# Optimization experiments

Measured on AMD Instinct MI355X. Metric: run time of the kernel, lower is better.

## Reference

```python
import jax, jax.numpy as jnp
import numpy as np

VOCAB, P, K, B, L, R = 50257, 512, 64, 32, 2048, 5


def setup_inputs() -> dict:
    key = jax.random.key(0)
    k1, k2, k3, k4, k5, k6, k7 = jax.random.split(key, 7)
    return {
        "x": jax.random.randint(k1, (B, L), 0, VOCAB, dtype=jnp.int32),
        "V": jax.random.normal(k2, (VOCAB, P), dtype=jnp.float32),
        "C": jax.random.normal(k3, (K, P), dtype=jnp.float32),
        "f1_w": jax.random.normal(k4, (2 * R + 1,), dtype=jnp.float32),
        "f1_b": jax.random.normal(k5, (K,), dtype=jnp.float32),
        "f2_w": jax.random.normal(k6, (K, P), dtype=jnp.float32),
        "f2_b": jax.random.normal(k7, (K,), dtype=jnp.float32),
    }


def reference(x, V, C, f1_w, f1_b, f2_w, f2_b):
    b, l = x.shape
    k, p = C.shape
    w = f1_w.shape[0]
    r = (w - 1) // 2
    emb = V[x]                                              # [B,L,P] embedding lookup
    x_hat = emb / jnp.linalg.norm(emb, axis=2, keepdims=True)
    l_hat = C / jnp.linalg.norm(C, axis=1, keepdims=True)
    G = jnp.einsum('kp,blp->bkl', l_hat, x_hat)             # cosine sim [B,K,L]
    # sliding-window dot product == depthwise 1D cross-correlation, 'same' padding
    u = jax.lax.conv_general_dilated(
        G.reshape(b * k, 1, l), f1_w.reshape(1, 1, w),
        window_strides=(1,), padding=[(r, r)],
        dimension_numbers=('NCH', 'OIH', 'NCH'),
    ).reshape(b, k, l)
    m = jax.nn.relu(u + f1_b[None, :, None])                # [B,K,L]
    beta = jax.nn.softmax(m.max(axis=1), axis=1)            # max over labels, softmax over seq -> [B,L]
    pooled = jnp.mean(beta[:, :, None] * emb, axis=1)       # [B,P]
    return pooled @ f2_w.T + f2_b                           # [B,K]
```

## Files before the change

kernel.cpp:

```cpp
#include <hip/hip_runtime.h>
#include <hip/hip_bf16.h>

#define PP     512
#define KK     64
#define BB     32
#define LLEN   2048
#define NPOS   (BB * LLEN)

typedef __attribute__((ext_vector_type(8)))  short short8;
typedef __attribute__((ext_vector_type(16))) float float16;

__device__ inline unsigned int pack_bf2(float lo, float hi) {
    __hip_bfloat162 h = __float22bfloat162_rn(make_float2(lo, hi));
    unsigned int u;
    __builtin_memcpy(&u, &h, 4);
    return u;
}
__device__ inline float bf_lo(unsigned int v) { return __uint_as_float(v << 16); }
__device__ inline float bf_hi(unsigned int v) { return __uint_as_float(v & 0xffff0000u); }

__global__ void k1_prep(const float* __restrict__ C, const float* __restrict__ f2w,
                        ushort* __restrict__ Bu) {
    const int n = blockIdx.x;
    const float* src = (n < 64) ? (C + n * PP) : (f2w + (n - 64) * PP);
    const int t = threadIdx.x;
    float v0 = src[t];
    float v1 = src[t + 256];
    __shared__ float red[256];
    red[t] = v0 * v0 + v1 * v1;
    __syncthreads();
    for (int s = 128; s > 0; s >>= 1) {
        if (t < s) red[t] += red[t + s];
        __syncthreads();
    }
    const float inv = (n < 64) ? rsqrtf(red[0]) : 1.f;
    Bu[(((t >> 3)      * 128 + n) << 3) + (t & 7)] = (ushort)(pack_bf2(v0 * inv, 0.f) & 0xffffu);
    Bu[((((t + 256) >> 3)) * 128 + n) * 8 + (t & 7)] = (ushort)(pack_bf2(v1 * inv, 0.f) & 0xffffu);
}

__launch_bounds__(256, 3)
__global__ void k2_gemm(const int* __restrict__ x, const float* __restrict__ V,
                        const uint4* __restrict__ Bu4,
                        unsigned int* __restrict__ Gt2, unsigned int* __restrict__ E2p) {
    __shared__ uint4 sA[64 * 16];
    __shared__ uint4 sB[16 * 128];
    __shared__ int   stok[64];
    __shared__ float rnorm[64];

    const int tid  = threadIdx.x;
    const int lane = tid & 63;
    const int wv   = tid >> 6;

    if (tid < 64) stok[tid] = x[blockIdx.x * 64 + tid];

    float16 acc0, acc1;
#pragma unroll
    for (int i = 0; i < 16; ++i) { acc0[i] = 0.f; acc1[i] = 0.f; }
    float nacc[4];
#pragma unroll
    for (int i = 0; i < 4; ++i) nacc[i] = 0.f;

    const int mt = (wv & 1) * 32;
    const int nh = (wv >> 1) * 64;

    for (int kc = 0; kc < 4; ++kc) {
        __syncthreads();
#pragma unroll
        for (int i = 0; i < 4; ++i) {
            const int m = (tid >> 4) + i * 16;
            const int f = tid & 15;
            const float* src = V + (size_t)stok[m] * PP + kc * 128 + f * 8;
            const float4 a = ((const float4*)src)[0];
            const float4 b = ((const float4*)src)[1];
            uint4 wq;
            wq.x = pack_bf2(a.x, a.y); wq.y = pack_bf2(a.z, a.w);
            wq.z = pack_bf2(b.x, b.y); wq.w = pack_bf2(b.z, b.w);
            sA[m * 16 + (f ^ (m & 7))] = wq;
            float s2 = 0.f;
            s2 = fmaf(a.x, a.x, s2); s2 = fmaf(a.y, a.y, s2);
            s2 = fmaf(a.z, a.z, s2); s2 = fmaf(a.w, a.w, s2);
            s2 = fmaf(b.x, b.x, s2); s2 = fmaf(b.y, b.y, s2);
            s2 = fmaf(b.z, b.z, s2); s2 = fmaf(b.w, b.w, s2);
            nacc[i] += s2;
        }
#pragma unroll
        for (int i = 0; i < 8; ++i)
            sB[i * 256 + tid] = Bu4[kc * 2048 + i * 256 + tid];

        if (kc == 3) {
#pragma unroll
            for (int i = 0; i < 4; ++i) {
                float r = nacc[i];
                r += __shfl_down(r, 8, 16);
                r += __shfl_down(r, 4, 16);
                r += __shfl_down(r, 2, 16);
                r += __shfl_down(r, 1, 16);
                if ((tid & 15) == 0) rnorm[(tid >> 4) + i * 16] = rsqrtf(r);
            }
        }
        __syncthreads();

#pragma unroll
        for (int kb = 0; kb < 8; ++kb) {
            const int f  = kb * 2 + (lane >> 5);
            const int mq = mt + (lane & 31);
            const uint4 av = sA[mq * 16 + (f ^ (mq & 7))];
            const uint4 b0 = sB[f * 128 + nh + (lane & 31)];
            const uint4 b1 = sB[f * 128 + nh + 32 + (lane & 31)];
            short8 a8, t0, t1;
            __builtin_memcpy(&a8, &av, 16);
            __builtin_memcpy(&t0, &b0, 16);
            __builtin_memcpy(&t1, &b1, 16);
            acc0 = __builtin_amdgcn_mfma_f32_32x32x16_bf16(a8, t0, acc0, 0, 0, 0);
            acc1 = __builtin_amdgcn_mfma_f32_32x32x16_bf16(a8, t1, acc1, 0, 0, 0);
        }
    }

    const size_t posBase = (size_t)blockIdx.x * 64;
#pragma unroll
    for (int reg = 0; reg < 16; ++reg) {
        const int r  = (reg & 3) + 8 * (reg >> 2) + 4 * (lane >> 5);
        const int mq = mt + r;
        const size_t p = posBase + mq;
        if (wv < 2) {
            const float rn = rnorm[mq];
            Gt2[p * 32 + (lane & 31)] = pack_bf2(acc0[reg] * rn, acc1[reg] * rn);
        } else {
            E2p[p * 32 + (lane & 31)] = pack_bf2(acc0[reg], acc1[reg]);
        }
    }
}

__global__ void k3_convmax(const unsigned int* __restrict__ Gt2, const float* __restrict__ f1w,
                           const float* __restrict__ f1b, float* __restrict__ mm) {
    __shared__ unsigned int sT[138 * 33];
    const int b  = blockIdx.x >> 4;
    const int l0 = (blockIdx.x & 15) * 128;
    const int t  = threadIdx.x;
    for (int idx = t; idx < 138 * 32; idx += 256) {
        const int row = idx >> 5, col = idx & 31;
        const int gl = l0 - 5 + row;
        sT[row * 33 + col] = (gl >= 0 && gl < LLEN)
            ? Gt2[((size_t)b * LLEN + gl) * 32 + col] : 0u;
    }
    __syncthreads();
    float w[11];
#pragma unroll
    for (int j = 0; j < 11; ++j) w[j] = f1w[j];
    const int j = t & 31;
    const int h = t >> 5;
    const float bias0 = f1b[j], bias1 = f1b[j + 32];
#pragma unroll 2
    for (int i = 0; i < 16; ++i) {
        const int lr = i * 8 + h;
        float u0 = 0.f, u1 = 0.f;
#pragma unroll
        for (int tap = 0; tap < 11; ++tap) {
            const unsigned int v = sT[(lr + tap) * 33 + j];
            u0 = fmaf(bf_lo(v), w[tap], u0);
            u1 = fmaf(bf_hi(v), w[tap], u1);
        }
        float m = fmaxf(fmaxf(u0 + bias0, 0.f), fmaxf(u1 + bias1, 0.f));
#pragma unroll
        for (int off = 16; off > 0; off >>= 1)
            m = fmaxf(m, __shfl_xor(m, off, 64));
        if (j == 0) mm[b * LLEN + l0 + lr] = m;
    }
}

__global__ void k7_softpool(const float* __restrict__ mm, const unsigned int* __restrict__ E2p,
                            const float* __restrict__ f2b, float* __restrict__ out) {
    const int b = blockIdx.x;
    const int t = threadIdx.x;
    __shared__ float red[256];
    __shared__ float sbeta[LLEN];
    __shared__ float sred[8][64];

    float v[8];
    float mx = -1e30f;
#pragma unroll
    for (int i = 0; i < 8; ++i) {
        v[i] = mm[b * LLEN + t + i * 256];
        mx = fmaxf(mx, v[i]);
    }
    red[t] = mx;
    __syncthreads();
    for (int s = 128; s > 0; s >>= 1) {
        if (t < s) red[t] = fmaxf(red[t], red[t + s]);
        __syncthreads();
    }
    mx = red[0];
    __syncthreads();
    float sm = 0.f;
#pragma unroll
    for (int i = 0; i < 8; ++i) {
        v[i] = __expf(v[i] - mx);
        sm += v[i];
    }
    red[t] = sm;
    __syncthreads();
    for (int s = 128; s > 0; s >>= 1) {
        if (t < s) red[t] += red[t + s];
        __syncthreads();
    }
    const float inv = 1.f / red[0];
#pragma unroll
    for (int i = 0; i < 8; ++i) sbeta[t + i * 256] = v[i] * inv;
    __syncthreads();

    const int j = t & 31, h = t >> 5;
    float a0 = 0.f, a1 = 0.f;
#pragma unroll 8
    for (int i = 0; i < 256; ++i) {
        const int l = i * 8 + h;
        const float wgt = sbeta[l];
        const unsigned int e = E2p[((size_t)b * LLEN + l) * 32 + j];
        a0 = fmaf(wgt, bf_lo(e), a0);
        a1 = fmaf(wgt, bf_hi(e), a1);
    }
    sred[h][j]      = a0;
    sred[h][j + 32] = a1;
    __syncthreads();
    if (t < 64) {
        float r = 0.f;
#pragma unroll
        for (int hh = 0; hh < 8; ++hh) r += sred[hh][t];
        out[b * KK + t] = r * (1.f / 2048.f) + f2b[t];
    }
}

extern "C" void kernel_launch(void* const* d_in, const int* in_sizes, int n_in,
                              void* d_out, int out_size, void* d_ws, size_t ws_size,
                              hipStream_t stream) {
    const int*   x   = (const int*)d_in[0];
    const float* V   = (const float*)d_in[1];
    const float* C   = (const float*)d_in[2];
    const float* f1w = (const float*)d_in[3];
    const float* f1b = (const float*)d_in[4];
    const float* f2w = (const float*)d_in[5];
    const float* f2b = (const float*)d_in[6];
    float* out = (float*)d_out;

    float* ws = (float*)d_ws;
    ushort* Bu = (ushort*)ws;
    unsigned int* Gt2 = (unsigned int*)(ws + 32768);
    unsigned int* E2p = Gt2 + (size_t)NPOS * 32;
    float* mm = (float*)(E2p + (size_t)NPOS * 32);

    k1_prep    <<<128, 256, 0, stream>>>(C, f2w, Bu);
    k2_gemm    <<<NPOS / 64, 256, 0, stream>>>(x, V, (const uint4*)Bu, Gt2, E2p);
    k3_convmax <<<BB * (LLEN / 128), 256, 0, stream>>>(Gt2, f1w, f1b, mm);
    k7_softpool<<<BB, 256, 0, stream>>>(mm, E2p, f2b, out);
}
```

Before: 200.6 us.

## Fuse softmax-pooling into conv kernel with split softmax and prefetch gather rows

The per-batch softmax and weighted pooling move into the conv/max kernel. Each 128-position chunk computes a local max, a local exp-sum and a partial pooled vector, and a small final kernel merges the chunks with rescaled online-softmax. This replaces the 32-block pooling kernel that streamed all of E2p serially with work spread over 512 blocks. The GEMM kernel also register-prefetches the next K-chunk of the gathered V rows before the MFMA loop, which overlaps the global gather with compute at the cost of extra registers.

```diff
diff --git a/kernel.cpp b/kernel.cpp
--- a/kernel.cpp
+++ b/kernel.cpp
@@ -34,7 +34,7 @@
         __syncthreads();
     }
     const float inv = (n < 64) ? rsqrtf(red[0]) : 1.f;
-    Bu[(((t >> 3)      * 128 + n) << 3) + (t & 7)] = (ushort)(pack_bf2(v0 * inv, 0.f) & 0xffffu);
+    Bu[(((t >> 3)       * 128 + n) << 3) + (t & 7)] = (ushort)(pack_bf2(v0 * inv, 0.f) & 0xffffu);
     Bu[((((t + 256) >> 3)) * 128 + n) * 8 + (t & 7)] = (ushort)(pack_bf2(v1 * inv, 0.f) & 0xffffu);
 }
 
@@ -50,8 +50,11 @@
     const int tid  = threadIdx.x;
     const int lane = tid & 63;
     const int wv   = tid >> 6;
+    const int f    = tid & 15;
+    const int mrow = tid >> 4;
 
     if (tid < 64) stok[tid] = x[blockIdx.x * 64 + tid];
+    __syncthreads();
 
     float16 acc0, acc1;
 #pragma unroll
@@ -63,15 +66,21 @@
     const int mt = (wv & 1) * 32;
     const int nh = (wv >> 1) * 64;
 
+    float4 pa[4][2];
+#pragma unroll
+    for (int i = 0; i < 4; ++i) {
+        const float* src = V + (size_t)stok[mrow + i * 16] * PP + f * 8;
+        pa[i][0] = ((const float4*)src)[0];
+        pa[i][1] = ((const float4*)src)[1];
+    }
+
     for (int kc = 0; kc < 4; ++kc) {
         __syncthreads();
 #pragma unroll
         for (int i = 0; i < 4; ++i) {
-            const int m = (tid >> 4) + i * 16;
-            const int f = tid & 15;
-            const float* src = V + (size_t)stok[m] * PP + kc * 128 + f * 8;
-            const float4 a = ((const float4*)src)[0];
-            const float4 b = ((const float4*)src)[1];
+            const int m = mrow + i * 16;
+            const float4 a = pa[i][0];
+            const float4 b = pa[i][1];
             uint4 wq;
             wq.x = pack_bf2(a.x, a.y); wq.y = pack_bf2(a.z, a.w);
             wq.z = pack_bf2(b.x, b.y); wq.w = pack_bf2(b.z, b.w);
@@ -87,7 +96,14 @@
         for (int i = 0; i < 8; ++i)
             sB[i * 256 + tid] = Bu4[kc * 2048 + i * 256 + tid];
 
-        if (kc == 3) {
+        if (kc < 3) {
+#pragma unroll
+            for (int i = 0; i < 4; ++i) {
+                const float* src = V + (size_t)stok[mrow + i * 16] * PP + (kc + 1) * 128 + f * 8;
+                pa[i][0] = ((const float4*)src)[0];
+                pa[i][1] = ((const float4*)src)[1];
+            }
+        } else {
 #pragma unroll
             for (int i = 0; i < 4; ++i) {
                 float r = nacc[i];
@@ -95,18 +111,18 @@
                 r += __shfl_down(r, 4, 16);
                 r += __shfl_down(r, 2, 16);
                 r += __shfl_down(r, 1, 16);
-                if ((tid & 15) == 0) rnorm[(tid >> 4) + i * 16] = rsqrtf(r);
+                if (f == 0) rnorm[mrow + i * 16] = rsqrtf(r);
             }
         }
         __syncthreads();
 
 #pragma unroll
         for (int kb = 0; kb < 8; ++kb) {
-            const int f  = kb * 2 + (lane >> 5);
+            const int ff = kb * 2 + (lane >> 5);
             const int mq = mt + (lane & 31);
-            const uint4 av = sA[mq * 16 + (f ^ (mq & 7))];
-            const uint4 b0 = sB[f * 128 + nh + (lane & 31)];
-            const uint4 b1 = sB[f * 128 + nh + 32 + (lane & 31)];
+            const uint4 av = sA[mq * 16 + (ff ^ (mq & 7))];
+            const uint4 b0 = sB[ff * 128 + nh + (lane & 31)];
+            const uint4 b1 = sB[ff * 128 + nh + 32 + (lane & 31)];
             short8 a8, t0, t1;
             __builtin_memcpy(&a8, &av, 16);
             __builtin_memcpy(&t0, &b0, 16);
@@ -131,12 +147,20 @@
     }
 }
 
-__global__ void k3_convmax(const unsigned int* __restrict__ Gt2, const float* __restrict__ f1w,
-                           const float* __restrict__ f1b, float* __restrict__ mm) {
+__global__ void k3_convpool(const unsigned int* __restrict__ Gt2,
+                            const unsigned int* __restrict__ E2p,
+                            const float* __restrict__ f1w, const float* __restrict__ f1b,
+                            float* __restrict__ pool) {
     __shared__ unsigned int sT[138 * 33];
+    __shared__ float smv[128];
+    __shared__ float sp[128];
+    __shared__ float sscal[2];
+    __shared__ float sred[8][64];
+
     const int b  = blockIdx.x >> 4;
     const int l0 = (blockIdx.x & 15) * 128;
     const int t  = threadIdx.x;
+
     for (int idx = t; idx < 138 * 32; idx += 256) {
         const int row = idx >> 5, col = idx & 31;
         const int gl = l0 - 5 + row;
@@ -144,6 +168,7 @@
             ? Gt2[((size_t)b * LLEN + gl) * 32 + col] : 0u;
     }
     __syncthreads();
+
     float w[11];
 #pragma unroll
     for (int j = 0; j < 11; ++j) w[j] = f1w[j];
@@ -164,57 +189,35 @@
 #pragma unroll
         for (int off = 16; off > 0; off >>= 1)
             m = fmaxf(m, __shfl_xor(m, off, 64));
-        if (j == 0) mm[b * LLEN + l0 + lr] = m;
-    }
-}
-
-__global__ void k7_softpool(const float* __restrict__ mm, const unsigned int* __restrict__ E2p,
-                            const float* __restrict__ f2b, float* __restrict__ out) {
-    const int b = blockIdx.x;
-    const int t = threadIdx.x;
-    __shared__ float red[256];
-    __shared__ float sbeta[LLEN];
-    __shared__ float sred[8][64];
-
-    float v[8];
-    float mx = -1e30f;
-#pragma unroll
-    for (int i = 0; i < 8; ++i) {
-        v[i] = mm[b * LLEN + t + i * 256];
-        mx = fmaxf(mx, v[i]);
-    }
-    red[t] = mx;
-    __syncthreads();
-    for (int s = 128; s > 0; s >>= 1) {
-        if (t < s) red[t] = fmaxf(red[t], red[t + s]);
-        __syncthreads();
-    }
-    mx = red[0];
-    __syncthreads();
-    float sm = 0.f;
-#pragma unroll
-    for (int i = 0; i < 8; ++i) {
-        v[i] = __expf(v[i] - mx);
-        sm += v[i];
-    }
-    red[t] = sm;
-    __syncthreads();
-    for (int s = 128; s > 0; s >>= 1) {
-        if (t < s) red[t] += red[t + s];
-        __syncthreads();
-    }
-    const float inv = 1.f / red[0];
-#pragma unroll
-    for (int i = 0; i < 8; ++i) sbeta[t + i * 256] = v[i] * inv;
-    __syncthreads();
-
-    const int j = t & 31, h = t >> 5;
+        if (j == 0) smv[lr] = m;
+    }
+    __syncthreads();
+
+    if (t < 64) {
+        float v = fmaxf(smv[t], smv[t + 64]);
+#pragma unroll
+        for (int off = 32; off > 0; off >>= 1)
+            v = fmaxf(v, __shfl_xor(v, off, 64));
+        if (t == 0) sscal[0] = v;
+    }
+    __syncthreads();
+    const float mx = sscal[0];
+    if (t < 128) sp[t] = __expf(smv[t] - mx);
+    __syncthreads();
+    if (t < 64) {
+        float s = sp[t] + sp[t + 64];
+#pragma unroll
+        for (int off = 32; off > 0; off >>= 1)
+            s += __shfl_xor(s, off, 64);
+        if (t == 0) sscal[1] = s;
+    }
+
     float a0 = 0.f, a1 = 0.f;
-#pragma unroll 8
-    for (int i = 0; i < 256; ++i) {
+#pragma unroll 4
+    for (int i = 0; i < 16; ++i) {
         const int l = i * 8 + h;
-        const float wgt = sbeta[l];
-        const unsigned int e = E2p[((size_t)b * LLEN + l) * 32 + j];
+        const float wgt = sp[l];
+        const unsigned int e = E2p[((size_t)b * LLEN + l0 + l) * 32 + j];
         a0 = fmaf(wgt, bf_lo(e), a0);
         a1 = fmaf(wgt, bf_hi(e), a1);
     }
@@ -225,8 +228,29 @@
         float r = 0.f;
 #pragma unroll
         for (int hh = 0; hh < 8; ++hh) r += sred[hh][t];
-        out[b * KK + t] = r * (1.f / 2048.f) + f2b[t];
-    }
+        float* dst = pool + (size_t)blockIdx.x * 68;
+        dst[t] = r;
+        if (t == 0) { dst[64] = mx; dst[65] = sscal[1]; }
+    }
+}
+
+__global__ void k6_final(const float* __restrict__ pool, const float* __restrict__ f2b,
+                         float* __restrict__ out) {
+    const int b = blockIdx.x;
+    const int k = threadIdx.x;
+    float M = -1e30f;
+#pragma unroll
+    for (int c = 0; c < 16; ++c)
+        M = fmaxf(M, pool[(size_t)(b * 16 + c) * 68 + 64]);
+    float tot = 0.f, num = 0.f;
+#pragma unroll
+    for (int c = 0; c < 16; ++c) {
+        const float* pc = pool + (size_t)(b * 16 + c) * 68;
+        const float sc = __expf(pc[64] - M);
+        tot = fmaf(sc, pc[65], tot);
+        num = fmaf(sc, pc[k], num);
+    }
+    out[b * KK + k] = (num / tot) * (1.f / 2048.f) + f2b[k];
 }
 
 extern "C" void kernel_launch(void* const* d_in, const int* in_sizes, int n_in,
@@ -245,10 +269,10 @@
     ushort* Bu = (ushort*)ws;
     unsigned int* Gt2 = (unsigned int*)(ws + 32768);
     unsigned int* E2p = Gt2 + (size_t)NPOS * 32;
-    float* mm = (float*)(E2p + (size_t)NPOS * 32);
+    float* pool = (float*)(E2p + (size_t)NPOS * 32);
 
     k1_prep    <<<128, 256, 0, stream>>>(C, f2w, Bu);
     k2_gemm    <<<NPOS / 64, 256, 0, stream>>>(x, V, (const uint4*)Bu, Gt2, E2p);
-    k3_convmax <<<BB * (LLEN / 128), 256, 0, stream>>>(Gt2, f1w, f1b, mm);
-    k7_softpool<<<BB, 256, 0, stream>>>(mm, E2p, f2b, out);
-}
+    k3_convpool<<<BB * 16, 256, 0, stream>>>(Gt2, E2p, f1w, f1b, pool);
+    k6_final   <<<BB, 64, 0, stream>>>(pool, f2b, out);
+}
```

New measurement: 209.5 us. +4.5%, slower.
